# Performance work log

Measured on AMD Instinct MI355X. Metric: run time of the kernel, lower is better.

Reference implementation:

```python
import jax, jax.numpy as jnp
import numpy as np

NHEAD = 16
HEAD_DIM = 64
ROPE_BASE = 10000.0


def _rotate_half(x):
    # interleaved convention: pairs (x0,x1)->(-x1,x0)
    x1 = x[..., ::2]
    x2 = x[..., 1::2]
    return jnp.stack([-x2, x1], axis=-1).reshape(x.shape)


def _rope_cache(seq_len, head_dim, base):
    half = head_dim // 2
    inv_freq = 1.0 / base ** (jnp.arange(half, dtype=jnp.float32) / float(half))
    t = jnp.arange(seq_len, dtype=jnp.float32)
    freqs = jnp.einsum('i,j->ij', t, inv_freq)          # [T, half]
    emb = jnp.concatenate([freqs, freqs], axis=-1)      # [T, D] (half-half cat, matches torch source)
    return jnp.cos(emb), jnp.sin(emb)


def setup_inputs() -> dict:
    key = jax.random.key(0)
    k1, k2, k3 = jax.random.split(key, 3)
    b, t, c = 2, 2048, 1024
    x = jax.random.normal(k1, (b, t, c), dtype=jnp.float32)
    # torch nn.Linear weights: [out_features, in_features], scaled like kaiming-uniform-ish
    W_qkv = jax.random.normal(k2, (3 * c, c), dtype=jnp.float32) / np.sqrt(c)
    W_out = jax.random.normal(k3, (c, c), dtype=jnp.float32) / np.sqrt(c)
    return {"x": x, "W_qkv": W_qkv, "W_out": W_out}


def reference(x, W_qkv, W_out):
    b, t, c = x.shape
    nh, hd = NHEAD, HEAD_DIM
    qkv = x @ W_qkv.T                                   # [b, t, 3c]
    q, k, v = jnp.split(qkv, 3, axis=-1)

    def to_heads(a):
        return a.reshape(b, t, nh, hd).transpose(0, 2, 1, 3)  # [b, nh, t, hd]

    q, k, v = to_heads(q), to_heads(k), to_heads(v)
    cos, sin = _rope_cache(t, hd, ROPE_BASE)            # [t, hd]
    cos = cos.astype(q.dtype)[None, None]
    sin = sin.astype(q.dtype)[None, None]
    q = q * cos + _rotate_half(q) * sin
    k = k * cos + _rotate_half(k) * sin

    scale = 1.0 / np.sqrt(hd).astype(np.float32)
    scores = jnp.einsum('bhqd,bhkd->bhqk', q, k) * scale
    attn = jax.nn.softmax(scores, axis=-1)
    y = jnp.einsum('bhqk,bhkd->bhqd', attn, v)          # [b, nh, t, hd]
    y = y.transpose(0, 2, 1, 3).reshape(b, t, c)
    return y @ W_out.T
```

## Files before the change

### kernel.cpp

```cpp
#include <hip/hip_runtime.h>
#include <hip/hip_bf16.h>
#include <math.h>

typedef __hip_bfloat16 bf16;
typedef _Float16 f16;
typedef __attribute__((ext_vector_type(8))) short bf16x8;
typedef __attribute__((ext_vector_type(8))) _Float16 f16x8;
typedef __attribute__((ext_vector_type(4))) float f32x4;

#define MFMA_BF(a,b,c) __builtin_amdgcn_mfma_f32_16x16x32_bf16((a),(b),(c),0,0,0)
#define MFMA_F16(a,b,c) __builtin_amdgcn_mfma_f32_16x16x32_f16((a),(b),(c),0,0,0)

__device__ __forceinline__ void load_lds16(const void* g, void* l) {
  __builtin_amdgcn_global_load_lds(
      (__attribute__((address_space(1))) void*)(g),
      (__attribute__((address_space(3))) void*)(l), 16, 0, 0);
}

__device__ __forceinline__ unsigned pk_bf16(float a, float b) {
  unsigned ua = __builtin_bit_cast(unsigned, a);
  unsigned ub = __builtin_bit_cast(unsigned, b);
  ua += 0x7fffu + ((ua >> 16) & 1u);
  ub += 0x7fffu + ((ub >> 16) & 1u);
  return (ua >> 16) | (ub & 0xffff0000u);
}

__global__ void cvt_all(const float* __restrict__ x, const float* __restrict__ wq,
                        const float* __restrict__ wo, unsigned* __restrict__ xb,
                        unsigned* __restrict__ wqb, unsigned* __restrict__ wob) {
  int i = blockIdx.x * blockDim.x + threadIdx.x;
  const float* src;
  unsigned* dst;
  int off;
  if (i < 1048576) { src = x; dst = xb; off = i; }
  else if (i < 1048576 + 786432) { src = wq; dst = wqb; off = i - 1048576; }
  else { src = wo; dst = wob; off = i - (1048576 + 786432); }
  float4 v = reinterpret_cast<const float4*>(src)[off];
  uint2 u;
  u.x = pk_bf16(v.x, v.y);
  u.y = pk_bf16(v.z, v.w);
  reinterpret_cast<uint2*>(dst)[off] = u;
}

__global__ __launch_bounds__(256, 2)
void gemm_qkv(const bf16* __restrict__ A, const bf16* __restrict__ B,
              bf16* __restrict__ outq, bf16* __restrict__ outk,
              f16* __restrict__ outv) {
  __shared__ __align__(16) bf16 As[128 * 32];
  __shared__ __align__(16) bf16 Bs[128 * 32];
  __shared__ __align__(16) f16 Ts[4][32 * 72];
  const int K = 1024;
  const int tid = threadIdx.x;
  const int w = tid >> 6;
  const int lane = tid & 63;
  const int quad = lane >> 4;
  const int col = lane & 15;
  const int waveM = w >> 1;
  const int waveN = w & 1;
  const int bm = blockIdx.y * 128;
  const int bn = blockIdx.x * 128;

  f32x4 acc[4][4] = {};
  const int srow = lane >> 2;
  const int skoff = (lane & 3) * 8;

  for (int k0 = 0; k0 < K; k0 += 32) {
    __syncthreads();
#pragma unroll
    for (int p = 0; p < 2; ++p) {
      int r = p * 64 + w * 16 + srow;
      load_lds16(A + (size_t)(bm + r) * K + k0 + skoff, (char*)As + p * 4096 + w * 1024);
      load_lds16(B + (size_t)(bn + r) * K + k0 + skoff, (char*)Bs + p * 4096 + w * 1024);
    }
    __syncthreads();
    bf16x8 af[4], bfr[4];
#pragma unroll
    for (int i = 0; i < 4; ++i)
      af[i] = *reinterpret_cast<const bf16x8*>(As + (waveM * 64 + i * 16 + col) * 32 + quad * 8);
#pragma unroll
    for (int j = 0; j < 4; ++j)
      bfr[j] = *reinterpret_cast<const bf16x8*>(Bs + (waveN * 64 + j * 16 + col) * 32 + quad * 8);
#pragma unroll
    for (int i = 0; i < 4; ++i)
#pragma unroll
      for (int j = 0; j < 4; ++j)
        acc[i][j] = MFMA_BF(af[i], bfr[j], acc[i][j]);
  }

  if (bn < 2048) {
    const float NEGK = -0.4152410118f;
    const float C1 = 0.1803368799f;
    const float sgn = (col & 1) ? 1.0f : -1.0f;
#pragma unroll
    for (int j = 0; j < 4; ++j) {
      const int n0 = bn + waveN * 64 + j * 16;
      const int sel = n0 >> 10;
      const int hh = (n0 & 1023) >> 6;
      const int dd = (n0 & 63) + col;
      bf16* outp = sel ? outk : outq;
      const float post = sel ? 1.0f : C1;
      const float invf = __builtin_amdgcn_exp2f((float)((n0 & 31) + col) * NEGK);
#pragma unroll
      for (int i = 0; i < 4; ++i) {
#pragma unroll
        for (int r = 0; r < 4; ++r) {
          int m = bm + waveM * 64 + i * 16 + quad * 4 + r;
          int b = m >> 11, t = m & 2047;
          float v = acc[i][j][r];
          float partner = __shfl_xor(v, 1);
          float ang = (float)t * invf;
          float res = (v * __cosf(ang) + sgn * partner * __sinf(ang)) * post;
          outp[((size_t)(b * 16 + hh) * 2048 + t) * 64 + dd] = __float2bfloat16(res);
        }
      }
    }
  } else {
    f16* tb = &Ts[w][0];
    const int nq = bn + waveN * 64;
    const int hh = (nq & 1023) >> 6;
    const int b = bm >> 11;
    const int tbase = (bm & 2047) + waveM * 64;
    f16* dst0 = outv + (size_t)(b * 16 + hh) * 64 * 2048;
#pragma unroll
    for (int jh = 0; jh < 2; ++jh) {
#pragma unroll
      for (int j2 = 0; j2 < 2; ++j2) {
        const int j = jh * 2 + j2;
        const int dl = j2 * 16 + col;
#pragma unroll
        for (int i = 0; i < 4; ++i)
#pragma unroll
          for (int r = 0; r < 4; ++r)
            tb[dl * 72 + i * 16 + quad * 4 + r] = (f16)acc[i][j][r];
      }
      __asm__ volatile("s_waitcnt lgkmcnt(0)" ::: "memory");
      const int dl = lane >> 1;
      const int thalf = (lane & 1) * 32;
#pragma unroll
      for (int rr = 0; rr < 4; ++rr) {
        f16x8 vrow = *reinterpret_cast<const f16x8*>(tb + dl * 72 + thalf + rr * 8);
        *reinterpret_cast<f16x8*>(dst0 + (size_t)(jh * 32 + dl) * 2048 + tbase + thalf + rr * 8) = vrow;
      }
      __asm__ volatile("s_waitcnt lgkmcnt(0)" ::: "memory");
    }
  }
}

__global__ __launch_bounds__(256, 2)
void gemm_out(const bf16* __restrict__ A, const bf16* __restrict__ B,
              float* __restrict__ outf) {
  __shared__ __align__(16) bf16 As[64 * 32];
  __shared__ __align__(16) bf16 Bs[128 * 32];
  const int K = 1024;
  const int tid = threadIdx.x;
  const int w = tid >> 6;
  const int lane = tid & 63;
  const int quad = lane >> 4;
  const int col = lane & 15;
  const int bm = blockIdx.y * 64;
  const int bn = blockIdx.x * 128;

  f32x4 acc[4][2] = {};
  const int srow = lane >> 2;
  const int skoff = (lane & 3) * 8;

  for (int k0 = 0; k0 < K; k0 += 32) {
    __syncthreads();
    load_lds16(A + (size_t)(bm + w * 16 + srow) * K + k0 + skoff, (char*)As + w * 1024);
#pragma unroll
    for (int p = 0; p < 2; ++p)
      load_lds16(B + (size_t)(bn + p * 64 + w * 16 + srow) * K + k0 + skoff,
                 (char*)Bs + p * 4096 + w * 1024);
    __syncthreads();
    bf16x8 af[4], bfr[2];
#pragma unroll
    for (int i = 0; i < 4; ++i)
      af[i] = *reinterpret_cast<const bf16x8*>(As + (i * 16 + col) * 32 + quad * 8);
#pragma unroll
    for (int j = 0; j < 2; ++j)
      bfr[j] = *reinterpret_cast<const bf16x8*>(Bs + (w * 32 + j * 16 + col) * 32 + quad * 8);
#pragma unroll
    for (int i = 0; i < 4; ++i)
#pragma unroll
      for (int j = 0; j < 2; ++j)
        acc[i][j] = MFMA_BF(af[i], bfr[j], acc[i][j]);
  }

#pragma unroll
  for (int i = 0; i < 4; ++i)
#pragma unroll
    for (int j = 0; j < 2; ++j) {
      const int n0 = bn + w * 32 + j * 16;
#pragma unroll
      for (int r = 0; r < 4; ++r) {
        int m = bm + i * 16 + quad * 4 + r;
        outf[(size_t)m * 1024 + n0 + col] = acc[i][j][r];
      }
    }
}

__global__ __launch_bounds__(256, 3)
void attn_kernel(const bf16* __restrict__ qh, const bf16* __restrict__ kh,
                 const f16* __restrict__ vt, bf16* __restrict__ O1,
                 bf16* __restrict__ O2, float* __restrict__ lw) {
  __shared__ __align__(16) bf16 Ks[2][64 * 64];
  __shared__ __align__(16) f16 Vs[2][64 * 64];
  __shared__ __align__(16) f16 Ps[4][32 * 72];

  const int bh = blockIdx.z;
  const int split = blockIdx.y;
  const int kc0 = split << 10;
  const int w = threadIdx.x >> 6;
  const int lane = threadIdx.x & 63;
  const int quad = lane >> 4;
  const int col = lane & 15;

  const int qrow0 = blockIdx.x * 128 + w * 32 + col;
  bf16x8 qf[2][2];
#pragma unroll
  for (int f = 0; f < 2; ++f)
#pragma unroll
    for (int c = 0; c < 2; ++c)
      qf[f][c] = *reinterpret_cast<const bf16x8*>(
          qh + ((size_t)bh * 2048 + qrow0 + f * 16) * 64 + c * 32 + quad * 8);

  const int s8 = lane >> 3;
  const int blk = (lane & 7) ^ s8;
  const bf16* kg = kh + (size_t)bh * 2048 * 64;
  const f16* vg = vt + (size_t)bh * 64 * 2048;
  char* klds0 = (char*)&Ks[0][0] + w * 2048;
  char* vlds0 = (char*)&Vs[0][0] + w * 2048;
  const int ksrc0 = s8 * 4 + w;
  const int ksrc1 = (8 + s8) * 4 + w;
  const int vrow0 = w * 16 + s8;

  const int csw = col & 7;
  const int sw0 = (quad ^ csw) * 8;
  const int sw1 = ((quad + 4) ^ csw) * 8;
  const int rdbase = col * 64;

  f32x4 O[2][4] = {};
  float l[2][4] = {};
  f16* ps = &Ps[w][0];

  load_lds16(kg + (size_t)(kc0 + ksrc0) * 64 + blk * 8, klds0);
  load_lds16(kg + (size_t)(kc0 + ksrc1) * 64 + blk * 8, klds0 + 1024);
  load_lds16(vg + (size_t)vrow0 * 2048 + kc0 + blk * 8, vlds0);
  load_lds16(vg + (size_t)(vrow0 + 8) * 2048 + kc0 + blk * 8, vlds0 + 1024);

  int buf = 0;
  const int kend = kc0 + 1024;
  for (int kc = kc0; kc < kend; kc += 64) {
    __asm__ volatile("s_waitcnt vmcnt(0)" ::: "memory");
    __asm__ volatile("s_barrier" ::: "memory");
    if (kc + 64 < kend) {
      const int nb = buf ^ 1;
      const int kn = kc + 64;
      load_lds16(kg + (size_t)(kn + ksrc0) * 64 + blk * 8, klds0 + nb * 8192);
      load_lds16(kg + (size_t)(kn + ksrc1) * 64 + blk * 8, klds0 + nb * 8192 + 1024);
      load_lds16(vg + (size_t)vrow0 * 2048 + kn + blk * 8, vlds0 + nb * 8192);
      load_lds16(vg + (size_t)(vrow0 + 8) * 2048 + kn + blk * 8, vlds0 + nb * 8192 + 1024);
    }

    const bf16* kt = &Ks[buf][0];
    const f16* vtile = &Vs[buf][0];

    f32x4 s[2][4];
#pragma unroll
    for (int t = 0; t < 4; ++t) {
      bf16x8 kf0 = *reinterpret_cast<const bf16x8*>(kt + t * 1024 + rdbase + sw0);
      bf16x8 kf1 = *reinterpret_cast<const bf16x8*>(kt + t * 1024 + rdbase + sw1);
#pragma unroll
      for (int f = 0; f < 2; ++f) {
        f32x4 a = {};
        a = MFMA_BF(qf[f][0], kf0, a);
        a = MFMA_BF(qf[f][1], kf1, a);
        s[f][t] = a;
      }
    }

#pragma unroll
    for (int f = 0; f < 2; ++f)
#pragma unroll
      for (int r = 0; r < 4; ++r) {
        float p0 = __builtin_amdgcn_exp2f(s[f][0][r]);
        float p1 = __builtin_amdgcn_exp2f(s[f][1][r]);
        float p2 = __builtin_amdgcn_exp2f(s[f][2][r]);
        float p3 = __builtin_amdgcn_exp2f(s[f][3][r]);
        l[f][r] += (p0 + p1) + (p2 + p3);
        uint2 w2;
        w2.x = __builtin_bit_cast(unsigned, __builtin_amdgcn_cvt_pkrtz(p0, p1));
        w2.y = __builtin_bit_cast(unsigned, __builtin_amdgcn_cvt_pkrtz(p2, p3));
        *reinterpret_cast<uint2*>((char*)ps + (f * 16 + quad * 4 + r) * 144 + col * 8) = w2;
      }
    __asm__ volatile("s_waitcnt lgkmcnt(0)" ::: "memory");

    f16x8 pf[2][2];
#pragma unroll
    for (int f = 0; f < 2; ++f) {
      pf[f][0] = *reinterpret_cast<const f16x8*>(ps + (f * 16 + col) * 72 + quad * 8);
      pf[f][1] = *reinterpret_cast<const f16x8*>(ps + (f * 16 + col) * 72 + 32 + quad * 8);
    }

#pragma unroll
    for (int j = 0; j < 4; ++j) {
      f16x8 vf0 = *reinterpret_cast<const f16x8*>(vtile + j * 1024 + rdbase + sw0);
      f16x8 vf1 = *reinterpret_cast<const f16x8*>(vtile + j * 1024 + rdbase + sw1);
#pragma unroll
      for (int f = 0; f < 2; ++f) {
        O[f][j] = MFMA_F16(pf[f][0], vf0, O[f][j]);
        O[f][j] = MFMA_F16(pf[f][1], vf1, O[f][j]);
      }
    }
    buf ^= 1;
  }

  bf16* o_out = split ? O2 : O1;
  float* lrow = lw + split * 65536 + bh * 2048;
  const int b = bh >> 4, h = bh & 15;
#pragma unroll
  for (int f = 0; f < 2; ++f)
#pragma unroll
    for (int r = 0; r < 4; ++r) {
      float lv = l[f][r];
#pragma unroll
      for (int off = 1; off < 16; off <<= 1)
        lv += __shfl_xor(lv, off, 64);
      int t = blockIdx.x * 128 + w * 32 + f * 16 + quad * 4 + r;
      if (col == 0) lrow[t] = lv;
      size_t base = ((size_t)b * 2048 + t) * 1024 + h * 64;
#pragma unroll
      for (int j = 0; j < 4; ++j)
        o_out[base + j * 16 + col] = __float2bfloat16(O[f][j][r]);
    }
}

__global__ void merge_y(const bf16* __restrict__ O1, const bf16* __restrict__ O2,
                        const float* __restrict__ lw, bf16* __restrict__ y) {
  int i = blockIdx.x * blockDim.x + threadIdx.x;
  int c8 = i & 127;
  int t = (i >> 7) & 2047;
  int b = i >> 18;
  int bh = b * 16 + (c8 >> 3);
  float inv = 1.0f / (lw[bh * 2048 + t] + lw[65536 + bh * 2048 + t]);
  size_t off = (size_t)i * 8;
  ushort4 a1 = *reinterpret_cast<const ushort4*>((const unsigned short*)O1 + off);
  ushort4 a2 = *reinterpret_cast<const ushort4*>((const unsigned short*)O2 + off);
  ushort4 b1 = *reinterpret_cast<const ushort4*>((const unsigned short*)O1 + off + 4);
  ushort4 b2 = *reinterpret_cast<const ushort4*>((const unsigned short*)O2 + off + 4);
  const unsigned short* u1 = &a1.x;
  const unsigned short* u2 = &a2.x;
  const unsigned short* v1 = &b1.x;
  const unsigned short* v2 = &b2.x;
  float o[8];
#pragma unroll
  for (int e = 0; e < 4; ++e) {
    float s1 = __builtin_bit_cast(float, (unsigned)u1[e] << 16) +
               __builtin_bit_cast(float, (unsigned)u2[e] << 16);
    float s2 = __builtin_bit_cast(float, (unsigned)v1[e] << 16) +
               __builtin_bit_cast(float, (unsigned)v2[e] << 16);
    o[e] = s1 * inv;
    o[e + 4] = s2 * inv;
  }
  uint4 res;
  res.x = pk_bf16(o[0], o[1]);
  res.y = pk_bf16(o[2], o[3]);
  res.z = pk_bf16(o[4], o[5]);
  res.w = pk_bf16(o[6], o[7]);
  *reinterpret_cast<uint4*>((unsigned short*)y + off) = res;
}

extern "C" void kernel_launch(void* const* d_in, const int* in_sizes, int n_in,
                              void* d_out, int out_size, void* d_ws, size_t ws_size,
                              hipStream_t stream) {
  const float* x    = (const float*)d_in[0];
  const float* wqkv = (const float*)d_in[1];
  const float* wout = (const float*)d_in[2];
  float* out = (float*)d_out;
  char* ws = (char*)d_ws;

  bf16* xb    = (bf16*)(ws);
  bf16* wqkvb = (bf16*)(ws + (size_t)(8 << 20));
  bf16* woutb = (bf16*)(ws + (size_t)(14 << 20));
  bf16* qh    = (bf16*)(ws + (size_t)(16 << 20));
  bf16* kh    = (bf16*)(ws + (size_t)(24 << 20));
  f16*  vt    = (f16*) (ws + (size_t)(32 << 20));
  bf16* O1    = (bf16*)(ws + (size_t)(40 << 20));
  bf16* O2    = (bf16*)(ws);
  float* lw   = (float*)(ws + (size_t)(8 << 20));
  bf16* y     = (bf16*)(ws + (size_t)(16 << 20));

  cvt_all<<<8192, 256, 0, stream>>>(x, wqkv, wout,
                                    (unsigned*)xb, (unsigned*)wqkvb, (unsigned*)woutb);
  gemm_qkv<<<dim3(24, 32), 256, 0, stream>>>(xb, wqkvb, qh, kh, vt);
  attn_kernel<<<dim3(16, 2, 32), 256, 0, stream>>>(qh, kh, vt, O1, O2, lw);
  merge_y<<<2048, 256, 0, stream>>>(O1, O2, lw, y);
  gemm_out<<<dim3(8, 64), 256, 0, stream>>>(y, woutb, out);
}
```

Baseline: 201.9 us.

## Swap MFMA operand order to keep P in registers, dropping LDS round trip

The attention kernel computes S^T by swapping the MFMA A/B operands, so each lane holds the scores for one query across consecutive keys. It then packs the exponentials directly into the f16 operand for the PV MFMA instead of staging P through shared memory. K rows are loaded in a permuted order so the key ordering matches the register layout. Removing the P buffer frees LDS, and occupancy is raised to 4 blocks. The output and row sums are now written as packed 4-element stores with a shorter shuffle reduction. Separately, the V projection epilogue writes transposed f16 directly with packed 8-byte stores instead of transposing through LDS, which trades coalescing for fewer LDS operations.

```diff
diff --git a/kernel.cpp b/kernel.cpp
--- a/kernel.cpp
+++ b/kernel.cpp
@@ -7,6 +7,7 @@
 typedef __attribute__((ext_vector_type(8))) short bf16x8;
 typedef __attribute__((ext_vector_type(8))) _Float16 f16x8;
 typedef __attribute__((ext_vector_type(4))) float f32x4;
+typedef __attribute__((ext_vector_type(4))) unsigned u32x4;
 
 #define MFMA_BF(a,b,c) __builtin_amdgcn_mfma_f32_16x16x32_bf16((a),(b),(c),0,0,0)
 #define MFMA_F16(a,b,c) __builtin_amdgcn_mfma_f32_16x16x32_f16((a),(b),(c),0,0,0)
@@ -48,7 +49,6 @@
               f16* __restrict__ outv) {
   __shared__ __align__(16) bf16 As[128 * 32];
   __shared__ __align__(16) bf16 Bs[128 * 32];
-  __shared__ __align__(16) f16 Ts[4][32 * 72];
   const int K = 1024;
   const int tid = threadIdx.x;
   const int w = tid >> 6;
@@ -115,33 +115,21 @@
       }
     }
   } else {
-    f16* tb = &Ts[w][0];
-    const int nq = bn + waveN * 64;
-    const int hh = (nq & 1023) >> 6;
     const int b = bm >> 11;
-    const int tbase = (bm & 2047) + waveM * 64;
-    f16* dst0 = outv + (size_t)(b * 16 + hh) * 64 * 2048;
-#pragma unroll
-    for (int jh = 0; jh < 2; ++jh) {
-#pragma unroll
-      for (int j2 = 0; j2 < 2; ++j2) {
-        const int j = jh * 2 + j2;
-        const int dl = j2 * 16 + col;
-#pragma unroll
-        for (int i = 0; i < 4; ++i)
-#pragma unroll
-          for (int r = 0; r < 4; ++r)
-            tb[dl * 72 + i * 16 + quad * 4 + r] = (f16)acc[i][j][r];
-      }
-      __asm__ volatile("s_waitcnt lgkmcnt(0)" ::: "memory");
-      const int dl = lane >> 1;
-      const int thalf = (lane & 1) * 32;
-#pragma unroll
-      for (int rr = 0; rr < 4; ++rr) {
-        f16x8 vrow = *reinterpret_cast<const f16x8*>(tb + dl * 72 + thalf + rr * 8);
-        *reinterpret_cast<f16x8*>(dst0 + (size_t)(jh * 32 + dl) * 2048 + tbase + thalf + rr * 8) = vrow;
-      }
-      __asm__ volatile("s_waitcnt lgkmcnt(0)" ::: "memory");
+    const int tt0 = (bm & 2047) + waveM * 64;
+#pragma unroll
+    for (int j = 0; j < 4; ++j) {
+      const int n0 = bn + waveN * 64 + j * 16;
+      const int hh = (n0 & 1023) >> 6;
+      const int dd = (n0 & 63) + col;
+      f16* dst = outv + (size_t)(b * 16 + hh) * 131072 + (size_t)dd * 2048;
+#pragma unroll
+      for (int i = 0; i < 4; ++i) {
+        uint2 pk;
+        pk.x = __builtin_bit_cast(unsigned, __builtin_amdgcn_cvt_pkrtz(acc[i][j][0], acc[i][j][1]));
+        pk.y = __builtin_bit_cast(unsigned, __builtin_amdgcn_cvt_pkrtz(acc[i][j][2], acc[i][j][3]));
+        *reinterpret_cast<uint2*>(dst + tt0 + i * 16 + quad * 4) = pk;
+      }
     }
   }
 }
@@ -199,13 +187,12 @@
     }
 }
 
-__global__ __launch_bounds__(256, 3)
+__global__ __launch_bounds__(256, 4)
 void attn_kernel(const bf16* __restrict__ qh, const bf16* __restrict__ kh,
                  const f16* __restrict__ vt, bf16* __restrict__ O1,
                  bf16* __restrict__ O2, float* __restrict__ lw) {
   __shared__ __align__(16) bf16 Ks[2][64 * 64];
   __shared__ __align__(16) f16 Vs[2][64 * 64];
-  __shared__ __align__(16) f16 Ps[4][32 * 72];
 
   const int bh = blockIdx.z;
   const int split = blockIdx.y;
@@ -230,8 +217,8 @@
   const f16* vg = vt + (size_t)bh * 64 * 2048;
   char* klds0 = (char*)&Ks[0][0] + w * 2048;
   char* vlds0 = (char*)&Vs[0][0] + w * 2048;
-  const int ksrc0 = s8 * 4 + w;
-  const int ksrc1 = (8 + s8) * 4 + w;
+  const int ks0 = 32 * (w >> 1) + 8 * ((4 * w + (s8 >> 2)) & 3) + 4 * (w & 1) + (s8 & 3);
+  const int ks1 = 32 * (w >> 1) + 8 * ((4 * w + 2 + (s8 >> 2)) & 3) + 4 * (w & 1) + (s8 & 3);
   const int vrow0 = w * 16 + s8;
 
   const int csw = col & 7;
@@ -240,11 +227,10 @@
   const int rdbase = col * 64;
 
   f32x4 O[2][4] = {};
-  float l[2][4] = {};
-  f16* ps = &Ps[w][0];
-
-  load_lds16(kg + (size_t)(kc0 + ksrc0) * 64 + blk * 8, klds0);
-  load_lds16(kg + (size_t)(kc0 + ksrc1) * 64 + blk * 8, klds0 + 1024);
+  float l[2] = {};
+
+  load_lds16(kg + (size_t)(kc0 + ks0) * 64 + blk * 8, klds0);
+  load_lds16(kg + (size_t)(kc0 + ks1) * 64 + blk * 8, klds0 + 1024);
   load_lds16(vg + (size_t)vrow0 * 2048 + kc0 + blk * 8, vlds0);
   load_lds16(vg + (size_t)(vrow0 + 8) * 2048 + kc0 + blk * 8, vlds0 + 1024);
 
@@ -256,8 +242,8 @@
     if (kc + 64 < kend) {
       const int nb = buf ^ 1;
       const int kn = kc + 64;
-      load_lds16(kg + (size_t)(kn + ksrc0) * 64 + blk * 8, klds0 + nb * 8192);
-      load_lds16(kg + (size_t)(kn + ksrc1) * 64 + blk * 8, klds0 + nb * 8192 + 1024);
+      load_lds16(kg + (size_t)(kn + ks0) * 64 + blk * 8, klds0 + nb * 8192);
+      load_lds16(kg + (size_t)(kn + ks1) * 64 + blk * 8, klds0 + nb * 8192 + 1024);
       load_lds16(vg + (size_t)vrow0 * 2048 + kn + blk * 8, vlds0 + nb * 8192);
       load_lds16(vg + (size_t)(vrow0 + 8) * 2048 + kn + blk * 8, vlds0 + nb * 8192 + 1024);
     }
@@ -273,33 +259,30 @@
 #pragma unroll
       for (int f = 0; f < 2; ++f) {
         f32x4 a = {};
-        a = MFMA_BF(qf[f][0], kf0, a);
-        a = MFMA_BF(qf[f][1], kf1, a);
+        a = MFMA_BF(kf0, qf[f][0], a);
+        a = MFMA_BF(kf1, qf[f][1], a);
         s[f][t] = a;
       }
     }
 
-#pragma unroll
-    for (int f = 0; f < 2; ++f)
-#pragma unroll
-      for (int r = 0; r < 4; ++r) {
-        float p0 = __builtin_amdgcn_exp2f(s[f][0][r]);
-        float p1 = __builtin_amdgcn_exp2f(s[f][1][r]);
-        float p2 = __builtin_amdgcn_exp2f(s[f][2][r]);
-        float p3 = __builtin_amdgcn_exp2f(s[f][3][r]);
-        l[f][r] += (p0 + p1) + (p2 + p3);
-        uint2 w2;
-        w2.x = __builtin_bit_cast(unsigned, __builtin_amdgcn_cvt_pkrtz(p0, p1));
-        w2.y = __builtin_bit_cast(unsigned, __builtin_amdgcn_cvt_pkrtz(p2, p3));
-        *reinterpret_cast<uint2*>((char*)ps + (f * 16 + quad * 4 + r) * 144 + col * 8) = w2;
-      }
-    __asm__ volatile("s_waitcnt lgkmcnt(0)" ::: "memory");
-
     f16x8 pf[2][2];
 #pragma unroll
     for (int f = 0; f < 2; ++f) {
-      pf[f][0] = *reinterpret_cast<const f16x8*>(ps + (f * 16 + col) * 72 + quad * 8);
-      pf[f][1] = *reinterpret_cast<const f16x8*>(ps + (f * 16 + col) * 72 + 32 + quad * 8);
+      unsigned pk[8];
+      float lf = 0.0f;
+#pragma unroll
+      for (int t = 0; t < 4; ++t) {
+        float p0 = __builtin_amdgcn_exp2f(s[f][t][0]);
+        float p1 = __builtin_amdgcn_exp2f(s[f][t][1]);
+        float p2 = __builtin_amdgcn_exp2f(s[f][t][2]);
+        float p3 = __builtin_amdgcn_exp2f(s[f][t][3]);
+        lf += (p0 + p1) + (p2 + p3);
+        pk[t * 2]     = __builtin_bit_cast(unsigned, __builtin_amdgcn_cvt_pkrtz(p0, p1));
+        pk[t * 2 + 1] = __builtin_bit_cast(unsigned, __builtin_amdgcn_cvt_pkrtz(p2, p3));
+      }
+      l[f] += lf;
+      pf[f][0] = __builtin_bit_cast(f16x8, (u32x4){pk[0], pk[1], pk[2], pk[3]});
+      pf[f][1] = __builtin_bit_cast(f16x8, (u32x4){pk[4], pk[5], pk[6], pk[7]});
     }
 
 #pragma unroll
@@ -308,8 +291,8 @@
       f16x8 vf1 = *reinterpret_cast<const f16x8*>(vtile + j * 1024 + rdbase + sw1);
 #pragma unroll
       for (int f = 0; f < 2; ++f) {
-        O[f][j] = MFMA_F16(pf[f][0], vf0, O[f][j]);
-        O[f][j] = MFMA_F16(pf[f][1], vf1, O[f][j]);
+        O[f][j] = MFMA_F16(vf0, pf[f][0], O[f][j]);
+        O[f][j] = MFMA_F16(vf1, pf[f][1], O[f][j]);
       }
     }
     buf ^= 1;
@@ -319,20 +302,21 @@
   float* lrow = lw + split * 65536 + bh * 2048;
   const int b = bh >> 4, h = bh & 15;
 #pragma unroll
-  for (int f = 0; f < 2; ++f)
-#pragma unroll
-    for (int r = 0; r < 4; ++r) {
-      float lv = l[f][r];
-#pragma unroll
-      for (int off = 1; off < 16; off <<= 1)
-        lv += __shfl_xor(lv, off, 64);
-      int t = blockIdx.x * 128 + w * 32 + f * 16 + quad * 4 + r;
-      if (col == 0) lrow[t] = lv;
-      size_t base = ((size_t)b * 2048 + t) * 1024 + h * 64;
-#pragma unroll
-      for (int j = 0; j < 4; ++j)
-        o_out[base + j * 16 + col] = __float2bfloat16(O[f][j][r]);
-    }
+  for (int f = 0; f < 2; ++f) {
+    float lv = l[f];
+    lv += __shfl_xor(lv, 16, 64);
+    lv += __shfl_xor(lv, 32, 64);
+    int tq = blockIdx.x * 128 + w * 32 + f * 16 + col;
+    if (lane < 16) lrow[tq] = lv;
+    size_t base = ((size_t)b * 2048 + tq) * 1024 + h * 64;
+#pragma unroll
+    for (int j = 0; j < 4; ++j) {
+      uint2 pk2;
+      pk2.x = pk_bf16(O[f][j][0], O[f][j][1]);
+      pk2.y = pk_bf16(O[f][j][2], O[f][j][3]);
+      *reinterpret_cast<uint2*>((unsigned short*)o_out + base + j * 16 + quad * 4) = pk2;
+    }
+  }
 }
 
 __global__ void merge_y(const bf16* __restrict__ O1, const bf16* __restrict__ O2,
```

Measured after the change: 198.4 us. No clear change (-1.7%).
